# Performance work log

Hardware: AMD Instinct MI355X
Metric: run time of the kernel (lower is better)

Reference implementation:

```python
import jax, jax.numpy as jnp
import numpy as np

NUM_CLASS = 1000
DIMS = 2048
NUM_HEADS = 8
HEAD = DIMS // NUM_HEADS  # 256
ALPHA = 0.999
N = 16384


def setup_inputs() -> dict:
    key = jax.random.key(0)
    k1, k2, k3 = jax.random.split(key, 3)
    x = jax.random.normal(k1, (N, DIMS), dtype=jnp.float32)
    labels = jax.random.randint(k2, (N,), 0, NUM_CLASS)
    centers = jax.random.normal(k3, (NUM_CLASS, NUM_HEADS, HEAD), dtype=jnp.float32)
    return {"x": x, "labels": labels, "centers": centers}


def reference(x, labels, centers):
    # gather per-sample centers: [N, H, hd]
    c = centers[labels]
    xh = x.reshape(-1, NUM_HEADS, HEAD)  # [N, H, hd]
    # per-head MSE, sum over heads, mean over batch
    loss = jnp.mean(jnp.square(xh - c), axis=-1).sum(axis=-1).mean()
    new_centers = centers.at[labels].set(ALPHA * c + (1.0 - ALPHA) * xh)
    return loss, new_centers
```

## Files before the change

kernel.cpp:

```cpp
#include <hip/hip_runtime.h>

#define NUM_CLASS 1000
#define DIMS 2048
#define NBATCH 16384
#define ALPHA 0.999f
#define LOSS_SCALE (1.0f / (16384.0f * 256.0f))

#define BLOCK 256
#define NBLOCKS 4096
#define ROWS_PER_BLOCK (NBATCH / NBLOCKS)

typedef float vfloat4 __attribute__((ext_vector_type(4)));

#define WS_LAST_INTS 1024

__global__ __launch_bounds__(BLOCK) void loss_kernel(
    const float* __restrict__ x,
    const int* __restrict__ labels,
    const float* __restrict__ centers,
    int* __restrict__ last,
    float* __restrict__ partials) {
    __shared__ float smf[4];
    const int tid  = threadIdx.x;
    const int lane = tid & 63;
    const int wid  = tid >> 6;
    const int row0 = blockIdx.x * ROWS_PER_BLOCK;

    if (tid < ROWS_PER_BLOCK) {
        const int row = row0 + tid;
        atomicMax(&last[labels[row]], row);
    }

    float acc = 0.0f;
    #pragma unroll
    for (int r = 0; r < ROWS_PER_BLOCK; ++r) {
        const int row   = row0 + r;
        const int label = labels[row];
        const vfloat4* xr = reinterpret_cast<const vfloat4*>(x + (size_t)row * DIMS);
        const vfloat4* cr = reinterpret_cast<const vfloat4*>(centers + (size_t)label * DIMS);
        #pragma unroll
        for (int j = 0; j < DIMS / 4 / BLOCK; ++j) {
            const int e = j * BLOCK + tid;
            vfloat4 xv = xr[e];
            vfloat4 cv = cr[e];
            vfloat4 d = xv - cv;
            acc += d.x * d.x + d.y * d.y + d.z * d.z + d.w * d.w;
        }
    }
    #pragma unroll
    for (int off = 32; off > 0; off >>= 1)
        acc += __shfl_down(acc, off, 64);
    if (lane == 0) smf[wid] = acc;
    __syncthreads();
    if (tid == 0)
        partials[blockIdx.x] = (smf[0] + smf[1]) + (smf[2] + smf[3]);
}

__global__ __launch_bounds__(BLOCK) void update_kernel(
    const float* __restrict__ x,
    const float* __restrict__ centers,
    const int* __restrict__ last,
    const float* __restrict__ partials,
    float* __restrict__ out_loss,
    float* __restrict__ newc) {
    __shared__ float smf[4];
    const int b   = blockIdx.x;
    const int tid = threadIdx.x;

    if (b == NUM_CLASS) {
        float acc = 0.0f;
        #pragma unroll
        for (int i = 0; i < NBLOCKS / BLOCK; ++i)
            acc += partials[i * BLOCK + tid];
        const int lane = tid & 63;
        const int wid  = tid >> 6;
        #pragma unroll
        for (int off = 32; off > 0; off >>= 1)
            acc += __shfl_down(acc, off, 64);
        if (lane == 0) smf[wid] = acc;
        __syncthreads();
        if (tid == 0)
            *out_loss = ((smf[0] + smf[1]) + (smf[2] + smf[3])) * LOSS_SCALE;
        return;
    }

    int li = last[b];
    if (li >= NBATCH) li = -1;

    const vfloat4* crow = reinterpret_cast<const vfloat4*>(centers + (size_t)b * DIMS);
    float* orow = newc + (size_t)b * DIMS;
    if (li >= 0) {
        const vfloat4* xrow = reinterpret_cast<const vfloat4*>(x + (size_t)li * DIMS);
        #pragma unroll
        for (int j = 0; j < DIMS / 4 / BLOCK; ++j) {
            const int e = j * BLOCK + tid;
            vfloat4 c4 = crow[e];
            vfloat4 x4 = xrow[e];
            float* o = orow + (size_t)e * 4;
            __builtin_nontemporal_store(ALPHA * c4.x + (1.0f - ALPHA) * x4.x, o + 0);
            __builtin_nontemporal_store(ALPHA * c4.y + (1.0f - ALPHA) * x4.y, o + 1);
            __builtin_nontemporal_store(ALPHA * c4.z + (1.0f - ALPHA) * x4.z, o + 2);
            __builtin_nontemporal_store(ALPHA * c4.w + (1.0f - ALPHA) * x4.w, o + 3);
        }
    } else {
        #pragma unroll
        for (int j = 0; j < DIMS / 4 / BLOCK; ++j) {
            const int e = j * BLOCK + tid;
            vfloat4 c4 = crow[e];
            float* o = orow + (size_t)e * 4;
            __builtin_nontemporal_store(c4.x, o + 0);
            __builtin_nontemporal_store(c4.y, o + 1);
            __builtin_nontemporal_store(c4.z, o + 2);
            __builtin_nontemporal_store(c4.w, o + 3);
        }
    }
}

extern "C" void kernel_launch(void* const* d_in, const int* in_sizes, int n_in,
                              void* d_out, int out_size, void* d_ws, size_t ws_size,
                              hipStream_t stream) {
    const float* x       = (const float*)d_in[0];
    const int*   labels  = (const int*)d_in[1];
    const float* centers = (const float*)d_in[2];

    float* out_loss = (float*)d_out;
    float* out_newc = (float*)d_out + 1;

    int*   last     = (int*)d_ws;
    float* partials = (float*)d_ws + WS_LAST_INTS;

    loss_kernel<<<NBLOCKS, BLOCK, 0, stream>>>(x, labels, centers, last, partials);
    update_kernel<<<NUM_CLASS + 1, BLOCK, 0, stream>>>(x, centers, last, partials,
                                                       out_loss, out_newc);
}
```

Before: 203.6 us.

## Fuse loss and EMA update into one cooperative kernel with grid sync

```diff
diff --git a/kernel.cpp b/kernel.cpp
--- a/kernel.cpp
+++ b/kernel.cpp
@@ -1,4 +1,7 @@
 #include <hip/hip_runtime.h>
+#include <hip/hip_cooperative_groups.h>
+
+namespace cg = cooperative_groups;
 
 #define NUM_CLASS 1000
 #define DIMS 2048
@@ -7,24 +10,27 @@
 #define LOSS_SCALE (1.0f / (16384.0f * 256.0f))
 
 #define BLOCK 256
-#define NBLOCKS 4096
-#define ROWS_PER_BLOCK (NBATCH / NBLOCKS)
+#define GRID 1024
+#define ROWS_PER_BLOCK (NBATCH / GRID)
 
 typedef float vfloat4 __attribute__((ext_vector_type(4)));
 
 #define WS_LAST_INTS 1024
 
-__global__ __launch_bounds__(BLOCK) void loss_kernel(
+__global__ __launch_bounds__(BLOCK) void fused_kernel(
     const float* __restrict__ x,
     const int* __restrict__ labels,
     const float* __restrict__ centers,
     int* __restrict__ last,
-    float* __restrict__ partials) {
+    float* __restrict__ partials,
+    float* __restrict__ out_loss,
+    float* __restrict__ newc) {
     __shared__ float smf[4];
     const int tid  = threadIdx.x;
     const int lane = tid & 63;
     const int wid  = tid >> 6;
-    const int row0 = blockIdx.x * ROWS_PER_BLOCK;
+    const int b    = blockIdx.x;
+    const int row0 = b * ROWS_PER_BLOCK;
 
     if (tid < ROWS_PER_BLOCK) {
         const int row = row0 + tid;
@@ -32,7 +38,6 @@
     }
 
     float acc = 0.0f;
-    #pragma unroll
     for (int r = 0; r < ROWS_PER_BLOCK; ++r) {
         const int row   = row0 + r;
         const int label = labels[row];
@@ -53,36 +58,26 @@
     if (lane == 0) smf[wid] = acc;
     __syncthreads();
     if (tid == 0)
-        partials[blockIdx.x] = (smf[0] + smf[1]) + (smf[2] + smf[3]);
-}
+        partials[b] = (smf[0] + smf[1]) + (smf[2] + smf[3]);
 
-__global__ __launch_bounds__(BLOCK) void update_kernel(
-    const float* __restrict__ x,
-    const float* __restrict__ centers,
-    const int* __restrict__ last,
-    const float* __restrict__ partials,
-    float* __restrict__ out_loss,
-    float* __restrict__ newc) {
-    __shared__ float smf[4];
-    const int b   = blockIdx.x;
-    const int tid = threadIdx.x;
+    __threadfence();
+    cg::this_grid().sync();
 
     if (b == NUM_CLASS) {
-        float acc = 0.0f;
+        float a2 = 0.0f;
         #pragma unroll
-        for (int i = 0; i < NBLOCKS / BLOCK; ++i)
-            acc += partials[i * BLOCK + tid];
-        const int lane = tid & 63;
-        const int wid  = tid >> 6;
+        for (int i = 0; i < GRID / BLOCK; ++i)
+            a2 += partials[i * BLOCK + tid];
         #pragma unroll
         for (int off = 32; off > 0; off >>= 1)
-            acc += __shfl_down(acc, off, 64);
-        if (lane == 0) smf[wid] = acc;
+            a2 += __shfl_down(a2, off, 64);
+        if (lane == 0) smf[wid] = a2;
         __syncthreads();
         if (tid == 0)
             *out_loss = ((smf[0] + smf[1]) + (smf[2] + smf[3])) * LOSS_SCALE;
         return;
     }
+    if (b >= NUM_CLASS) return;
 
     int li = last[b];
     if (li >= NBATCH) li = -1;
@@ -129,7 +124,9 @@
     int*   last     = (int*)d_ws;
     float* partials = (float*)d_ws + WS_LAST_INTS;
 
-    loss_kernel<<<NBLOCKS, BLOCK, 0, stream>>>(x, labels, centers, last, partials);
-    update_kernel<<<NUM_CLASS + 1, BLOCK, 0, stream>>>(x, centers, last, partials,
-                                                       out_loss, out_newc);
+    void* args[] = {(void*)&x, (void*)&labels, (void*)&centers,
+                    (void*)&last, (void*)&partials, (void*)&out_loss,
+                    (void*)&out_newc};
+    (void)hipLaunchCooperativeKernel(reinterpret_cast<void*>(fused_kernel),
+                                     dim3(GRID), dim3(BLOCK), args, 0, stream);
 }
```

Result: slower. 474.8 us (+133.3%).
